# Kernel tuning notes

Hardware: AMD Instinct MI355X
Metric: run time of the kernel (lower is better)

Reference implementation:

```python
import jax, jax.numpy as jnp
import numpy as np

B, L, IN_DIM, D_MODEL = 4, 1024, 128, 256
MDIM = 2 * D_MODEL          # mamba_dim = 512 (must equal 2*d_model for shape consistency)
NL = 4                      # mamba_layers
DIN = 2 * MDIM              # d_inner (expand=2)
NST = 16                    # d_state
DTR = MDIM // 16            # dt_rank = 32
KC = 4                      # d_conv
EPS = 1e-5

# sinusoidal positional encoding buffer (deterministic)
_pos = np.arange(L, dtype=np.float32)[:, None]
_div = np.exp(np.arange(0, MDIM, 2, dtype=np.float32) * (-np.log(10000.0) / MDIM))
_pe = np.zeros((L, MDIM), dtype=np.float32)
_pe[:, 0::2] = np.sin(_pos * _div)
_pe[:, 1::2] = np.cos(_pos * _div)
PE = jnp.asarray(_pe)


def setup_inputs() -> dict:
    key = jax.random.key(0)
    ks = iter(jax.random.split(key, 64))
    rn = lambda shape, s=0.02: jax.random.normal(next(ks), shape, jnp.float32) * s
    inp = {
        "x": jax.random.normal(next(ks), (B, L, IN_DIM), jnp.float32),
        "rtg": jax.random.normal(next(ks), (B, L, 1), jnp.float32),
        "state_emb_w": rn((D_MODEL, IN_DIM)), "state_emb_b": jnp.zeros((D_MODEL,)),
        "reward_emb_w": rn((D_MODEL, 1)), "reward_emb_b": jnp.zeros((D_MODEL,)),
        "ln_w": jnp.ones((MDIM,)), "ln_b": jnp.zeros((MDIM,)),
        "in_proj_w": rn((NL, 2 * DIN, MDIM)),
        "conv_w": rn((NL, DIN, KC), 0.1), "conv_b": jnp.zeros((NL, DIN)),
        "x_proj_w": rn((NL, DTR + 2 * NST, DIN)),
        "dt_proj_w": rn((NL, DIN, DTR), 0.1), "dt_proj_b": jnp.full((NL, DIN), -2.0),
        "A_log": jnp.tile(jnp.log(jnp.arange(1, NST + 1, dtype=jnp.float32)), (NL, DIN, 1)),
        "D_param": jnp.ones((NL, DIN)),
        "out_proj_w": rn((NL, MDIM, DIN)),
        "norm_w": jnp.ones((NL, MDIM)), "norm_f_w": jnp.ones((MDIM,)),
        "so_w1": rn((MDIM // 2, MDIM)), "so_b1": jnp.zeros((MDIM // 2,)),
        "so_w2": rn((IN_DIM, MDIM // 2)), "so_b2": jnp.zeros((IN_DIM,)),
        "ro_w1": rn((MDIM // 2, MDIM)), "ro_b1": jnp.zeros((MDIM // 2,)),
        "ro_w2": rn((1, MDIM // 2)), "ro_b2": jnp.zeros((1,)),
    }
    return inp


def _rmsnorm(h, w):
    return h * jax.lax.rsqrt(jnp.mean(h * h, -1, keepdims=True) + EPS) * w


def _mamba(h, ipw, cw, cb, xpw, dpw, dpb, Alog, Dp, opw):
    # h: [B,L,MDIM]
    Ls = h.shape[1]
    xz = h @ ipw.T                                   # [B,L,2*DIN]
    xx, z = jnp.split(xz, 2, axis=-1)
    # causal depthwise conv, kernel KC, left pad KC-1
    xp = jnp.pad(xx, ((0, 0), (KC - 1, 0), (0, 0)))
    xc = cb + sum(cw[:, k] * xp[:, k:k + Ls, :] for k in range(KC))
    xc = jax.nn.silu(xc)                             # [B,L,DIN]
    dbc = xc @ xpw.T                                 # [B,L,DTR+2*NST]
    dt = jax.nn.softplus(dbc[..., :DTR] @ dpw.T + dpb)   # [B,L,DIN]
    Bm = dbc[..., DTR:DTR + NST]                     # [B,L,NST]
    Cm = dbc[..., DTR + NST:]                        # [B,L,NST]
    A = -jnp.exp(Alog)                               # [DIN,NST]

    def step(hc, inp):
        dt_t, B_t, C_t, x_t = inp                    # [B,DIN],[B,NST],[B,NST],[B,DIN]
        hc = jnp.exp(dt_t[:, :, None] * A) * hc + (dt_t * x_t)[:, :, None] * B_t[:, None, :]
        return hc, jnp.einsum('bdn,bn->bd', hc, C_t)

    h0 = jnp.zeros((h.shape[0], DIN, NST), h.dtype)
    _, ys = jax.lax.scan(step, h0, (dt.swapaxes(0, 1), Bm.swapaxes(0, 1),
                                    Cm.swapaxes(0, 1), xc.swapaxes(0, 1)))
    y = ys.swapaxes(0, 1) + Dp * xc
    y = y * jax.nn.silu(z)
    return y @ opw.T                                 # [B,L,MDIM]


def _forward(x, rtg, state_emb_w, state_emb_b, reward_emb_w, reward_emb_b, ln_w, ln_b,
             in_proj_w, conv_w, conv_b, x_proj_w, dt_proj_w, dt_proj_b, A_log, D_param,
             out_proj_w, norm_w, norm_f_w, so_w1, so_b1, so_w2, so_b2, ro_w1, ro_b1, ro_w2, ro_b2):
    se = x @ state_emb_w.T + state_emb_b            # [B,L,D_MODEL]
    re = rtg @ reward_emb_w.T + reward_emb_b        # [B,L,D_MODEL]
    h = jnp.concatenate([se, re], axis=-1)          # [B,L,MDIM]
    h = h + PE[:h.shape[1]]                          # dropout is identity at eval
    mu = jnp.mean(h, -1, keepdims=True)
    var = jnp.var(h, -1, keepdims=True)
    h = (h - mu) * jax.lax.rsqrt(var + EPS) * ln_w + ln_b
    residual = None
    for i in range(NL):
        residual = h if residual is None else h + residual
        hn = _rmsnorm(residual, norm_w[i])
        h = _mamba(hn, in_proj_w[i], conv_w[i], conv_b[i], x_proj_w[i],
                   dt_proj_w[i], dt_proj_b[i], A_log[i], D_param[i], out_proj_w[i])
    residual = h + residual
    h = _rmsnorm(residual, norm_f_w)
    next_state = jax.nn.relu(h @ so_w1.T + so_b1) @ so_w2.T + so_b2   # [B,L,IN_DIM]
    next_reward = jax.nn.relu(h @ ro_w1.T + ro_b1) @ ro_w2.T + ro_b2  # [B,L,1]
    return next_state, next_reward


def reference(x, rtg, state_emb_w, state_emb_b, reward_emb_w, reward_emb_b, ln_w, ln_b,
              in_proj_w, conv_w, conv_b, x_proj_w, dt_proj_w, dt_proj_b, A_log, D_param,
              out_proj_w, norm_w, norm_f_w, so_w1, so_b1, so_w2, so_b2, ro_w1, ro_b1, ro_w2, ro_b2):
    return _forward(x, rtg, state_emb_w, state_emb_b, reward_emb_w, reward_emb_b, ln_w, ln_b,
                    in_proj_w, conv_w, conv_b, x_proj_w, dt_proj_w, dt_proj_b, A_log, D_param,
                    out_proj_w, norm_w, norm_f_w, so_w1, so_b1, so_w2, so_b2, ro_w1, ro_b1, ro_w2, ro_b2)
```

## Files before the change

### kernel.cpp

```cpp
#include <hip/hip_runtime.h>
#include <stdint.h>

typedef unsigned short u16;
typedef __attribute__((ext_vector_type(8))) short bf16x8;
typedef __attribute__((ext_vector_type(4))) float f32x4;

static __device__ __forceinline__ u16 f2b(float f) {
  uint32_t u = __builtin_bit_cast(uint32_t, f);
  u += 0x7fffu + ((u >> 16) & 1u);
  return (u16)(u >> 16);
}
static __device__ __forceinline__ float b2f(u16 h) {
  uint32_t u = ((uint32_t)h) << 16;
  return __builtin_bit_cast(float, u);
}

#define GLDS16(gsrc, ldst)                                                        \
  __builtin_amdgcn_global_load_lds(                                               \
      (const __attribute__((address_space(1))) void*)(gsrc),                      \
      (__attribute__((address_space(3))) void*)(ldst), 16, 0, 0)

__global__ void f2b_kernel(const float* __restrict__ in, u16* __restrict__ out, int n) {
  int i = blockIdx.x * 256 + threadIdx.x;
  if (i < n) out[i] = f2b(in[i]);
}

__global__ __launch_bounds__(256) void pe_kernel(float* __restrict__ PEt) {
  const int l = blockIdx.x;
  const float c = -9.210340371976184f / 512.f;
#pragma unroll
  for (int q = 0; q < 2; ++q) {
    int dd = threadIdx.x + q * 256;
    float div = expf((float)(2 * (dd >> 1)) * c);
    float v = (dd & 1) ? cosf((float)l * div) : sinf((float)l * div);
    PEt[(size_t)l * 512 + dd] = v;
  }
}

__global__ __launch_bounds__(256) void dpw_t_kernel(const float* __restrict__ dpw,
                                                    float* __restrict__ dpwT) {
  const int l = blockIdx.y;
  int idx = blockIdx.x * 256 + threadIdx.x;
  int j = idx >> 10, dd = idx & 1023;
  dpwT[(size_t)l * 32768 + idx] = dpw[(size_t)l * 32768 + (size_t)dd * 32 + j];
}

__global__ __launch_bounds__(256) void embed_ln2(
    const float* __restrict__ x, const float* __restrict__ rtg,
    const float* __restrict__ Wse, const float* __restrict__ bse,
    const float* __restrict__ Wre, const float* __restrict__ bre,
    const float* __restrict__ lnw, const float* __restrict__ lnb,
    const float* __restrict__ PEt, float* __restrict__ h) {
  const int tid = threadIdx.x;
  const int tok0 = blockIdx.x * 16;
  const int l0 = tok0 & 1023;
  __shared__ float xs[16][128];
  __shared__ float rt[16];
  __shared__ float sw[16][2][4];
  for (int i = tid; i < 16 * 128; i += 256) ((float*)xs)[i] = x[(size_t)tok0 * 128 + i];
  if (tid < 16) rt[tid] = rtg[tok0 + tid];
  __syncthreads();
  const int d = tid;
  float acc[16];
#pragma unroll
  for (int tt = 0; tt < 16; ++tt) acc[tt] = 0.f;
  const float* wrow = Wse + (size_t)d * 128;
  for (int k0 = 0; k0 < 128; k0 += 8) {
    float4 wa = *(const float4*)(wrow + k0);
    float4 wb = *(const float4*)(wrow + k0 + 4);
#pragma unroll
    for (int tt = 0; tt < 16; ++tt) {
      const float* xr = &xs[tt][k0];
      acc[tt] += xr[0] * wa.x + xr[1] * wa.y + xr[2] * wa.z + xr[3] * wa.w +
                 xr[4] * wb.x + xr[5] * wb.y + xr[6] * wb.z + xr[7] * wb.w;
    }
  }
  const float seb = bse[d], reW = Wre[d], reB = bre[d];
  const int lane = tid & 63, wv = tid >> 6;
  float h1a[16];
#pragma unroll
  for (int tt = 0; tt < 16; ++tt) {
    float h0 = acc[tt] + seb + PEt[(size_t)(l0 + tt) * 512 + d];
    float h1 = reB + rt[tt] * reW + PEt[(size_t)(l0 + tt) * 512 + 256 + d];
    acc[tt] = h0;
    h1a[tt] = h1;
    float s = h0 + h1, q = h0 * h0 + h1 * h1;
#pragma unroll
    for (int o = 32; o; o >>= 1) { s += __shfl_xor(s, o); q += __shfl_xor(q, o); }
    if (lane == 0) { sw[tt][0][wv] = s; sw[tt][1][wv] = q; }
  }
  __syncthreads();
#pragma unroll
  for (int tt = 0; tt < 16; ++tt) {
    float S = sw[tt][0][0] + sw[tt][0][1] + sw[tt][0][2] + sw[tt][0][3];
    float Q = sw[tt][1][0] + sw[tt][1][1] + sw[tt][1][2] + sw[tt][1][3];
    float mean = S * (1.f / 512.f);
    float var = Q * (1.f / 512.f) - mean * mean;
    float rstd = rsqrtf(var + 1e-5f);
    size_t base = (size_t)(tok0 + tt) * 512;
    h[base + d]       = (acc[tt] - mean) * rstd * lnw[d] + lnb[d];
    h[base + 256 + d] = (h1a[tt] - mean) * rstd * lnw[256 + d] + lnb[256 + d];
  }
}

__global__ __launch_bounds__(256) void resid_rms_kernel(
    const float* __restrict__ hin, float* __restrict__ residual,
    const float* __restrict__ w, u16* __restrict__ outb, int first) {
  const int tok = blockIdx.x;
  const int t = threadIdx.x;
  __shared__ float rq[4];
  size_t base = (size_t)tok * 512;
  float v0 = hin[base + t], v1 = hin[base + t + 256];
  if (!first) { v0 += residual[base + t]; v1 += residual[base + t + 256]; }
  residual[base + t] = v0;
  residual[base + t + 256] = v1;
  float q = v0 * v0 + v1 * v1;
#pragma unroll
  for (int o = 32; o; o >>= 1) q += __shfl_xor(q, o);
  if ((t & 63) == 0) rq[t >> 6] = q;
  __syncthreads();
  float Q = rq[0] + rq[1] + rq[2] + rq[3];
  float scale = rsqrtf(Q * (1.f / 512.f) + 1e-5f);
  outb[base + t]       = f2b(v0 * scale * w[t]);
  outb[base + t + 256] = f2b(v1 * scale * w[t + 256]);
}

template <int BM, int BN, int WM, int WN, int EPI>
__global__ __launch_bounds__(256) void gemm_bt(
    const u16* __restrict__ A, const u16* __restrict__ Bw,
    float* __restrict__ Cf, u16* __restrict__ Cb,
    const float* __restrict__ bias, int M, int N, int K) {
  constexpr int MF = BM / (WM * 16);
  constexpr int NF = BN / (WN * 16);
  constexpr int NCA = (BM * 4) / 256;
  constexpr int NCB = (BN * 4) / 256;
  __shared__ __align__(16) u16 lA[BM * 32];
  __shared__ __align__(16) u16 lB[BN * 32];
  const int tid = threadIdx.x;
  const int lane = tid & 63;
  const int wv = tid >> 6;
  const int wr = wv / WN, wc = wv % WN;
  const int m0 = blockIdx.x * BM, n0 = blockIdx.y * BN;
  const int kchunk = K / gridDim.z;
  const int kb = blockIdx.z * kchunk;

  f32x4 acc[MF][NF];
#pragma unroll
  for (int i = 0; i < MF; ++i)
#pragma unroll
    for (int j = 0; j < NF; ++j) acc[i][j] = (f32x4){0.f, 0.f, 0.f, 0.f};

  const int srow = tid >> 2, sck = tid & 3;
  const u16* Ag = A + (size_t)(m0 + srow) * K + sck * 8 + kb;
  const u16* Bg = Bw + (size_t)(n0 + srow) * K + sck * 8 + kb;

  for (int k0 = 0; k0 < kchunk; k0 += 32) {
#pragma unroll
    for (int it = 0; it < NCA; ++it)
      GLDS16(Ag + (size_t)it * 64 * K + k0, &lA[(it * 256 + tid) * 8]);
#pragma unroll
    for (int it = 0; it < NCB; ++it)
      GLDS16(Bg + (size_t)it * 64 * K + k0, &lB[(it * 256 + tid) * 8]);
    __syncthreads();
    bf16x8 af[MF], bfr[NF];
    const int koff = (lane >> 4) * 8;
#pragma unroll
    for (int mi = 0; mi < MF; ++mi) {
      int r = wr * (MF * 16) + mi * 16 + (lane & 15);
      af[mi] = *(const bf16x8*)(&lA[r * 32 + koff]);
    }
#pragma unroll
    for (int ni = 0; ni < NF; ++ni) {
      int r = wc * (NF * 16) + ni * 16 + (lane & 15);
      bfr[ni] = *(const bf16x8*)(&lB[r * 32 + koff]);
    }
#pragma unroll
    for (int mi = 0; mi < MF; ++mi)
#pragma unroll
      for (int ni = 0; ni < NF; ++ni)
        acc[mi][ni] = __builtin_amdgcn_mfma_f32_16x16x32_bf16(af[mi], bfr[ni], acc[mi][ni], 0, 0, 0);
    __syncthreads();
  }

  float* co = Cf + (size_t)blockIdx.z * (size_t)M * N;
  const int rbase = (lane >> 4) * 4;
  const int cbase = lane & 15;
#pragma unroll
  for (int mi = 0; mi < MF; ++mi) {
#pragma unroll
    for (int ni = 0; ni < NF; ++ni) {
      int row = m0 + wr * (MF * 16) + mi * 16 + rbase;
      int col = n0 + wc * (NF * 16) + ni * 16 + cbase;
      float bv = (EPI >= 2) ? bias[col] : 0.f;
#pragma unroll
      for (int r = 0; r < 4; ++r) {
        float v = acc[mi][ni][r] + bv;
        if (EPI == 2) v = fmaxf(v, 0.f);
        size_t idx = (size_t)(row + r) * N + col;
        if (EPI == 1 || EPI == 2) Cb[idx] = f2b(v);
        else co[idx] = v;
      }
    }
  }
}

__global__ __launch_bounds__(256) void conv_silu_kernel(
    const u16* __restrict__ xz, const float* __restrict__ cw,
    const float* __restrict__ cb, float* __restrict__ xc, u16* __restrict__ xcb) {
  int idx = blockIdx.x * 256 + threadIdx.x;
  int d = idx & 1023;
  int t = (idx >> 10) & 1023;
  int token = idx >> 10;
  float4 w4 = *(const float4*)(cw + (size_t)d * 4);
  const float wk[4] = {w4.x, w4.y, w4.z, w4.w};
  float s = cb[d];
  const u16* xx = xz + (size_t)(token - t) * 2048 + d;
#pragma unroll
  for (int k = 0; k < 4; ++k) {
    int tt = t - 3 + k;
    if (tt >= 0) s += wk[k] * b2f(xx[(size_t)tt * 2048]);
  }
  float sl = s / (1.f + expf(-s));
  xc[idx] = sl;
  xcb[idx] = f2b(sl);
}

__global__ __launch_bounds__(256) void dt_kernel2(
    const float* __restrict__ P, const float* __restrict__ dpwT,
    const float* __restrict__ dpb, float* __restrict__ dtout,
    float* __restrict__ dbcr) {
  const int tid = threadIdx.x;
  const int tok0 = blockIdx.x * 16;
  __shared__ float sm[16][64];
  const size_t str = (size_t)4096 * 64;
  for (int i = tid; i < 16 * 64; i += 256) {
    size_t o = (size_t)tok0 * 64 + i;
    float v = P[o] + P[str + o] + P[2 * str + o] + P[3 * str + o];
    ((float*)sm)[i] = v;
    dbcr[o] = v;
  }
  __syncthreads();
  float acc0[16], acc1[16], acc2[16], acc3[16];
#pragma unroll
  for (int t = 0; t < 16; ++t) { acc0[t] = 0.f; acc1[t] = 0.f; acc2[t] = 0.f; acc3[t] = 0.f; }
#pragma unroll 4
  for (int j = 0; j < 32; ++j) {
    float w0 = dpwT[(size_t)j * 1024 + tid];
    float w1 = dpwT[(size_t)j * 1024 + 256 + tid];
    float w2 = dpwT[(size_t)j * 1024 + 512 + tid];
    float w3 = dpwT[(size_t)j * 1024 + 768 + tid];
#pragma unroll
    for (int t = 0; t < 16; ++t) {
      float sv = sm[t][j];
      acc0[t] += sv * w0;
      acc1[t] += sv * w1;
      acc2[t] += sv * w2;
      acc3[t] += sv * w3;
    }
  }
  const float b0 = dpb[tid], b1 = dpb[256 + tid], b2 = dpb[512 + tid], b3 = dpb[768 + tid];
#pragma unroll
  for (int t = 0; t < 16; ++t) {
    size_t o = (size_t)(tok0 + t) * 1024 + tid;
    float a0 = acc0[t] + b0, a1 = acc1[t] + b1, a2 = acc2[t] + b2, a3 = acc3[t] + b3;
    dtout[o]       = (a0 > 20.f) ? a0 : logf(1.f + expf(a0));
    dtout[o + 256] = (a1 > 20.f) ? a1 : logf(1.f + expf(a1));
    dtout[o + 512] = (a2 > 20.f) ? a2 : logf(1.f + expf(a2));
    dtout[o + 768] = (a3 > 20.f) ? a3 : logf(1.f + expf(a3));
  }
}

__global__ __launch_bounds__(256) void scan1(
    const float* __restrict__ dt, const float* __restrict__ xc,
    const float* __restrict__ dbc, const float* __restrict__ Alog,
    float* __restrict__ Ebuf, float* __restrict__ Ubuf, int NCc, int TCc) {
  const int d = blockIdx.x * 256 + threadIdx.x;
  const int c = blockIdx.y;
  const int b = blockIdx.z;
  const int t0 = c * TCc;
  __shared__ __align__(16) float sB[64][16];
  for (int i = threadIdx.x; i < TCc * 16; i += 256) {
    int t = i >> 4, n = i & 15;
    sB[t][n] = dbc[((size_t)(b * 1024 + t0 + t)) * 64 + 32 + n];
  }
  float A2[16];
#pragma unroll
  for (int q = 0; q < 4; ++q) {
    float4 a4 = *(const float4*)(Alog + (size_t)d * 16 + q * 4);
    A2[q * 4 + 0] = -expf(a4.x) * 1.4426950408889634f;
    A2[q * 4 + 1] = -expf(a4.y) * 1.4426950408889634f;
    A2[q * 4 + 2] = -expf(a4.z) * 1.4426950408889634f;
    A2[q * 4 + 3] = -expf(a4.w) * 1.4426950408889634f;
  }
  __syncthreads();
  float hc[16];
#pragma unroll
  for (int n = 0; n < 16; ++n) hc[n] = 0.f;
  float sumdt = 0.f;
  size_t tok = (size_t)b * 1024 + t0;
  for (int t = 0; t < TCc; ++t, ++tok) {
    float dtv = dt[tok * 1024 + d];
    float xcv = xc[tok * 1024 + d];
    float du = dtv * xcv;
    sumdt += dtv;
#pragma unroll
    for (int q = 0; q < 4; ++q) {
      float4 B4 = *(const float4*)(&sB[t][q * 4]);
      float e0 = exp2f(dtv * A2[q * 4 + 0]);
      float e1 = exp2f(dtv * A2[q * 4 + 1]);
      float e2 = exp2f(dtv * A2[q * 4 + 2]);
      float e3 = exp2f(dtv * A2[q * 4 + 3]);
      hc[q * 4 + 0] = e0 * hc[q * 4 + 0] + du * B4.x;
      hc[q * 4 + 1] = e1 * hc[q * 4 + 1] + du * B4.y;
      hc[q * 4 + 2] = e2 * hc[q * 4 + 2] + du * B4.z;
      hc[q * 4 + 3] = e3 * hc[q * 4 + 3] + du * B4.w;
    }
  }
  size_t ob = (((size_t)b * NCc + c) * 16) * 1024 + d;
#pragma unroll
  for (int n = 0; n < 16; ++n) {
    Ebuf[ob + (size_t)n * 1024] = exp2f(A2[n] * sumdt);
    Ubuf[ob + (size_t)n * 1024] = hc[n];
  }
}

__global__ __launch_bounds__(256) void scan_mid(
    const float* __restrict__ Ebuf, const float* __restrict__ Ubuf,
    float* __restrict__ H0, int NCc) {
  int idx = blockIdx.x * 256 + threadIdx.x;
  int b = idx >> 14;
  int nd = idx & 16383;
  float h = 0.f;
  size_t o0 = ((size_t)b * NCc * 16) * 1024 + nd;
  const size_t cstr = (size_t)16 * 1024;
  for (int cc = 0; cc < NCc; ++cc) {
    size_t o = o0 + (size_t)cc * cstr;
    H0[o] = h;
    if (cc < NCc - 1) h = Ebuf[o] * h + Ubuf[o];
  }
}

__global__ __launch_bounds__(256) void scan2(
    const float* __restrict__ dt, const float* __restrict__ xc,
    const float* __restrict__ dbc, const u16* __restrict__ xz,
    const float* __restrict__ Alog, const float* __restrict__ Dp,
    const float* __restrict__ H0, u16* __restrict__ yg, int NCc, int TCc) {
  const int d = blockIdx.x * 256 + threadIdx.x;
  const int c = blockIdx.y;
  const int b = blockIdx.z;
  const int t0 = c * TCc;
  __shared__ __align__(16) float sB[64][16];
  __shared__ __align__(16) float sC[64][16];
  for (int i = threadIdx.x; i < TCc * 16; i += 256) {
    int t = i >> 4, n = i & 15;
    size_t o = ((size_t)(b * 1024 + t0 + t)) * 64 + 32;
    sB[t][n] = dbc[o + n];
    sC[t][n] = dbc[o + 16 + n];
  }
  float A2[16];
#pragma unroll
  for (int q = 0; q < 4; ++q) {
    float4 a4 = *(const float4*)(Alog + (size_t)d * 16 + q * 4);
    A2[q * 4 + 0] = -expf(a4.x) * 1.4426950408889634f;
    A2[q * 4 + 1] = -expf(a4.y) * 1.4426950408889634f;
    A2[q * 4 + 2] = -expf(a4.z) * 1.4426950408889634f;
    A2[q * 4 + 3] = -expf(a4.w) * 1.4426950408889634f;
  }
  const float Dd = Dp[d];
  float hc[16];
  size_t ob = (((size_t)b * NCc + c) * 16) * 1024 + d;
#pragma unroll
  for (int n = 0; n < 16; ++n) hc[n] = H0[ob + (size_t)n * 1024];
  __syncthreads();
  size_t tok = (size_t)b * 1024 + t0;
  for (int t = 0; t < TCc; ++t, ++tok) {
    float dtv = dt[tok * 1024 + d];
    float xcv = xc[tok * 1024 + d];
    float du = dtv * xcv;
    float y0 = 0.f, y1 = 0.f, y2 = 0.f, y3 = 0.f;
#pragma unroll
    for (int q = 0; q < 4; ++q) {
      float4 B4 = *(const float4*)(&sB[t][q * 4]);
      float4 C4 = *(const float4*)(&sC[t][q * 4]);
      float e0 = exp2f(dtv * A2[q * 4 + 0]);
      float e1 = exp2f(dtv * A2[q * 4 + 1]);
      float e2 = exp2f(dtv * A2[q * 4 + 2]);
      float e3 = exp2f(dtv * A2[q * 4 + 3]);
      hc[q * 4 + 0] = e0 * hc[q * 4 + 0] + du * B4.x;
      hc[q * 4 + 1] = e1 * hc[q * 4 + 1] + du * B4.y;
      hc[q * 4 + 2] = e2 * hc[q * 4 + 2] + du * B4.z;
      hc[q * 4 + 3] = e3 * hc[q * 4 + 3] + du * B4.w;
      y0 += hc[q * 4 + 0] * C4.x;
      y1 += hc[q * 4 + 1] * C4.y;
      y2 += hc[q * 4 + 2] * C4.z;
      y3 += hc[q * 4 + 3] * C4.w;
    }
    float y = (y0 + y1) + (y2 + y3);
    float z = b2f(xz[tok * 2048 + 1024 + d]);
    float g = z / (1.f + expf(-z));
    yg[tok * 1024 + d] = f2b((y + Dd * xcv) * g);
  }
}

__global__ __launch_bounds__(256) void reward_head_kernel(
    const u16* __restrict__ t1r, const float* __restrict__ w2,
    const float* __restrict__ b2, float* __restrict__ outr) {
  int tok = blockIdx.x * 4 + (threadIdx.x >> 6);
  int lane = threadIdx.x & 63;
  float s = 0.f;
#pragma unroll
  for (int j = 0; j < 256; j += 64) s += b2f(t1r[(size_t)tok * 256 + j + lane]) * w2[j + lane];
#pragma unroll
  for (int o = 32; o; o >>= 1) s += __shfl_xor(s, o);
  if (lane == 0) outr[tok] = s + b2[0];
}

extern "C" void kernel_launch(void* const* d_in, const int* in_sizes, int n_in,
                              void* d_out, int out_size, void* d_ws, size_t ws_size,
                              hipStream_t stream) {
  const float* x    = (const float*)d_in[0];
  const float* rtg  = (const float*)d_in[1];
  const float* Wse  = (const float*)d_in[2];
  const float* bse  = (const float*)d_in[3];
  const float* Wre  = (const float*)d_in[4];
  const float* bre  = (const float*)d_in[5];
  const float* lnw  = (const float*)d_in[6];
  const float* lnb  = (const float*)d_in[7];
  const float* ipw  = (const float*)d_in[8];
  const float* cw   = (const float*)d_in[9];
  const float* cb   = (const float*)d_in[10];
  const float* xpw  = (const float*)d_in[11];
  const float* dpw  = (const float*)d_in[12];
  const float* dpb  = (const float*)d_in[13];
  const float* Alog = (const float*)d_in[14];
  const float* Dp   = (const float*)d_in[15];
  const float* opw  = (const float*)d_in[16];
  const float* nw   = (const float*)d_in[17];
  const float* nfw  = (const float*)d_in[18];
  const float* sow1 = (const float*)d_in[19];
  const float* sob1 = (const float*)d_in[20];
  const float* sow2 = (const float*)d_in[21];
  const float* sob2 = (const float*)d_in[22];
  const float* row1 = (const float*)d_in[23];
  const float* rob1 = (const float*)d_in[24];
  const float* row2 = (const float*)d_in[25];
  const float* rob2 = (const float*)d_in[26];
  (void)in_sizes; (void)n_in; (void)out_size;

  char* wsp = (char*)d_ws;
  size_t off = 0;
  auto alloc = [&](size_t bytes) -> void* {
    off = (off + 255) & ~(size_t)255;
    void* p = wsp + off;
    off += bytes;
    return p;
  };
  const int TOK = 4096;
  float* h     = (float*)alloc((size_t)TOK * 512 * 4);
  float* resid = (float*)alloc((size_t)TOK * 512 * 4);
  u16* hn      = (u16*)alloc((size_t)TOK * 512 * 2);
  u16* xzb     = (u16*)alloc((size_t)TOK * 2048 * 2);
  float* xcf   = (float*)alloc((size_t)TOK * 1024 * 4);
  u16* xcb     = (u16*)alloc((size_t)TOK * 1024 * 2);
  float* dbcP  = (float*)alloc((size_t)4 * TOK * 64 * 4);
  float* dbc   = (float*)alloc((size_t)TOK * 64 * 4);
  float* dtf   = (float*)alloc((size_t)TOK * 1024 * 4);
  float* PEt   = (float*)alloc((size_t)1024 * 512 * 4);
  float* dpwT  = (float*)alloc((size_t)4 * 32 * 1024 * 4);
  u16* ipwb    = (u16*)alloc((size_t)4 * 2048 * 512 * 2);
  u16* xpwb    = (u16*)alloc((size_t)4 * 64 * 1024 * 2);
  u16* opwb    = (u16*)alloc((size_t)4 * 512 * 1024 * 2);
  u16* sow1b   = (u16*)alloc((size_t)256 * 512 * 2);
  u16* sow2b   = (u16*)alloc((size_t)128 * 256 * 2);
  u16* row1b   = (u16*)alloc((size_t)256 * 512 * 2);

  size_t base_off = (off + 255) & ~(size_t)255;
  auto scan_bytes = [](int nc) {
    return (size_t)3 * 4 * nc * 16 * 1024 * 4 + 512;
  };
  int NCc = 16;
  if (ws_size >= base_off + scan_bytes(64)) NCc = 64;
  else if (ws_size >= base_off + scan_bytes(32)) NCc = 32;
  int TCc = 1024 / NCc;
  char* shared8 = (char*)alloc((size_t)2 * 4096 * NCc * 16 * 4);
  float* Ebuf  = (float*)shared8;
  float* Ubuf  = Ebuf + (size_t)4096 * NCc * 16;
  float* H0    = (float*)alloc((size_t)4096 * NCc * 16 * 4);
  u16* t1s     = (u16*)shared8;
  u16* t1r     = t1s + (size_t)TOK * 256;

  auto cvt = [&](const float* src, u16* dst, int n) {
    f2b_kernel<<<(n + 255) / 256, 256, 0, stream>>>(src, dst, n);
  };
  cvt(ipw, ipwb, 4 * 2048 * 512);
  cvt(xpw, xpwb, 4 * 64 * 1024);
  cvt(opw, opwb, 4 * 512 * 1024);
  cvt(sow1, sow1b, 256 * 512);
  cvt(sow2, sow2b, 128 * 256);
  cvt(row1, row1b, 256 * 512);

  pe_kernel<<<1024, 256, 0, stream>>>(PEt);
  dpw_t_kernel<<<dim3(128, 4), 256, 0, stream>>>(dpw, dpwT);
  embed_ln2<<<256, 256, 0, stream>>>(x, rtg, Wse, bse, Wre, bre, lnw, lnb, PEt, h);

  for (int i = 0; i < 4; ++i) {
    resid_rms_kernel<<<TOK, 256, 0, stream>>>(h, resid, nw + i * 512, hn, i == 0);
    gemm_bt<128, 128, 2, 2, 1><<<dim3(32, 16, 1), 256, 0, stream>>>(
        hn, ipwb + (size_t)i * 2048 * 512, nullptr, xzb, nullptr, 4096, 2048, 512);
    conv_silu_kernel<<<TOK * 1024 / 256, 256, 0, stream>>>(
        xzb, cw + (size_t)i * 4096, cb + i * 1024, xcf, xcb);
    gemm_bt<128, 64, 2, 2, 0><<<dim3(32, 1, 4), 256, 0, stream>>>(
        xcb, xpwb + (size_t)i * 64 * 1024, dbcP, nullptr, nullptr, 4096, 64, 1024);
    dt_kernel2<<<TOK / 16, 256, 0, stream>>>(dbcP, dpwT + (size_t)i * 32 * 1024,
                                             dpb + i * 1024, dtf, dbc);
    scan1<<<dim3(4, NCc - 1, 4), 256, 0, stream>>>(
        dtf, xcf, dbc, Alog + (size_t)i * 1024 * 16, Ebuf, Ubuf, NCc, TCc);
    scan_mid<<<256, 256, 0, stream>>>(Ebuf, Ubuf, H0, NCc);
    scan2<<<dim3(4, NCc, 4), 256, 0, stream>>>(
        dtf, xcf, dbc, xzb, Alog + (size_t)i * 1024 * 16, Dp + i * 1024,
        H0, xcb, NCc, TCc);
    gemm_bt<128, 64, 2, 2, 0><<<dim3(32, 8, 1), 256, 0, stream>>>(
        xcb, opwb + (size_t)i * 512 * 1024, h, nullptr, nullptr, 4096, 512, 1024);
  }

  resid_rms_kernel<<<TOK, 256, 0, stream>>>(h, resid, nfw, hn, 0);
  gemm_bt<64, 64, 2, 2, 2><<<dim3(64, 4, 1), 256, 0, stream>>>(
      hn, sow1b, nullptr, t1s, sob1, 4096, 256, 512);
  gemm_bt<64, 64, 2, 2, 3><<<dim3(64, 2, 1), 256, 0, stream>>>(
      t1s, sow2b, (float*)d_out, nullptr, sob2, 4096, 128, 256);
  gemm_bt<64, 64, 2, 2, 2><<<dim3(64, 4, 1), 256, 0, stream>>>(
      hn, row1b, nullptr, t1r, rob1, 4096, 256, 512);
  reward_head_kernel<<<TOK / 4, 256, 0, stream>>>(
      t1r, row2, rob2, (float*)d_out + (size_t)TOK * 128);
}
```

Measured before the change: 721.0 us.

## Store dt and conv output in bf16, recompute chunk decay, vectorize conv, merge casts

The dt and conv/SiLU activations are now stored only as bf16. The fp32 xc and dt buffers are gone, and both scan kernels read the bf16 versions, which roughly halves their per-token activation traffic. scan1 no longer writes a per-state decay buffer; it writes one sum of dt per chunk, and scan_mid recomputes the exponential from A_log. The conv kernel processes 8 channels per thread with vector loads and stores, and the six weight-conversion launches are merged into one kernel. In exchange, dt and the scan input lose precision, and scan2 now reads and writes the same bf16 buffer in place.

```diff
diff --git a/kernel.cpp b/kernel.cpp
--- a/kernel.cpp
+++ b/kernel.cpp
@@ -3,6 +3,7 @@
 
 typedef unsigned short u16;
 typedef __attribute__((ext_vector_type(8))) short bf16x8;
+typedef __attribute__((ext_vector_type(8))) u16 u16x8;
 typedef __attribute__((ext_vector_type(4))) float f32x4;
 
 static __device__ __forceinline__ u16 f2b(float f) {
@@ -20,9 +21,21 @@
       (const __attribute__((address_space(1))) void*)(gsrc),                      \
       (__attribute__((address_space(3))) void*)(ldst), 16, 0, 0)
 
-__global__ void f2b_kernel(const float* __restrict__ in, u16* __restrict__ out, int n) {
+__global__ __launch_bounds__(256) void cvt6_kernel(
+    const float* __restrict__ a0, u16* __restrict__ b0,
+    const float* __restrict__ a1, u16* __restrict__ b1,
+    const float* __restrict__ a2, u16* __restrict__ b2,
+    const float* __restrict__ a3, u16* __restrict__ b3,
+    const float* __restrict__ a4, u16* __restrict__ b4,
+    const float* __restrict__ a5, u16* __restrict__ b5) {
   int i = blockIdx.x * 256 + threadIdx.x;
-  if (i < n) out[i] = f2b(in[i]);
+  const int n0 = 4194304, n1 = 262144, n2 = 2097152, n3 = 131072, n4 = 32768, n5 = 131072;
+  if (i < n0) { b0[i] = f2b(a0[i]); return; } i -= n0;
+  if (i < n1) { b1[i] = f2b(a1[i]); return; } i -= n1;
+  if (i < n2) { b2[i] = f2b(a2[i]); return; } i -= n2;
+  if (i < n3) { b3[i] = f2b(a3[i]); return; } i -= n3;
+  if (i < n4) { b4[i] = f2b(a4[i]); return; } i -= n4;
+  if (i < n5) { b5[i] = f2b(a5[i]); }
 }
 
 __global__ __launch_bounds__(256) void pe_kernel(float* __restrict__ PEt) {
@@ -204,30 +217,38 @@
   }
 }
 
-__global__ __launch_bounds__(256) void conv_silu_kernel(
+__global__ __launch_bounds__(256) void conv_silu_kernel2(
     const u16* __restrict__ xz, const float* __restrict__ cw,
-    const float* __restrict__ cb, float* __restrict__ xc, u16* __restrict__ xcb) {
-  int idx = blockIdx.x * 256 + threadIdx.x;
-  int d = idx & 1023;
-  int t = (idx >> 10) & 1023;
-  int token = idx >> 10;
-  float4 w4 = *(const float4*)(cw + (size_t)d * 4);
-  const float wk[4] = {w4.x, w4.y, w4.z, w4.w};
-  float s = cb[d];
-  const u16* xx = xz + (size_t)(token - t) * 2048 + d;
+    const float* __restrict__ cb, u16* __restrict__ xcb) {
+  int gid = blockIdx.x * 256 + threadIdx.x;
+  int d0 = (gid & 127) * 8;
+  int token = gid >> 7;
+  int t = token & 1023;
+  const u16* xx = xz + (size_t)(token - t) * 2048 + d0;
+  float s[8];
+#pragma unroll
+  for (int j = 0; j < 8; ++j) s[j] = cb[d0 + j];
 #pragma unroll
   for (int k = 0; k < 4; ++k) {
     int tt = t - 3 + k;
-    if (tt >= 0) s += wk[k] * b2f(xx[(size_t)tt * 2048]);
-  }
-  float sl = s / (1.f + expf(-s));
-  xc[idx] = sl;
-  xcb[idx] = f2b(sl);
+    if (tt >= 0) {
+      u16x8 v = *(const u16x8*)(xx + (size_t)tt * 2048);
+#pragma unroll
+      for (int j = 0; j < 8; ++j) s[j] += cw[(size_t)(d0 + j) * 4 + k] * b2f(v[j]);
+    }
+  }
+  u16x8 o;
+#pragma unroll
+  for (int j = 0; j < 8; ++j) {
+    float sl = s[j] / (1.f + expf(-s[j]));
+    o[j] = f2b(sl);
+  }
+  *(u16x8*)(xcb + (size_t)token * 1024 + d0) = o;
 }
 
 __global__ __launch_bounds__(256) void dt_kernel2(
     const float* __restrict__ P, const float* __restrict__ dpwT,
-    const float* __restrict__ dpb, float* __restrict__ dtout,
+    const float* __restrict__ dpb, u16* __restrict__ dtout,
     float* __restrict__ dbcr) {
   const int tid = threadIdx.x;
   const int tok0 = blockIdx.x * 16;
@@ -263,17 +284,17 @@
   for (int t = 0; t < 16; ++t) {
     size_t o = (size_t)(tok0 + t) * 1024 + tid;
     float a0 = acc0[t] + b0, a1 = acc1[t] + b1, a2 = acc2[t] + b2, a3 = acc3[t] + b3;
-    dtout[o]       = (a0 > 20.f) ? a0 : logf(1.f + expf(a0));
-    dtout[o + 256] = (a1 > 20.f) ? a1 : logf(1.f + expf(a1));
-    dtout[o + 512] = (a2 > 20.f) ? a2 : logf(1.f + expf(a2));
-    dtout[o + 768] = (a3 > 20.f) ? a3 : logf(1.f + expf(a3));
+    dtout[o]       = f2b((a0 > 20.f) ? a0 : logf(1.f + expf(a0)));
+    dtout[o + 256] = f2b((a1 > 20.f) ? a1 : logf(1.f + expf(a1)));
+    dtout[o + 512] = f2b((a2 > 20.f) ? a2 : logf(1.f + expf(a2)));
+    dtout[o + 768] = f2b((a3 > 20.f) ? a3 : logf(1.f + expf(a3)));
   }
 }
 
 __global__ __launch_bounds__(256) void scan1(
-    const float* __restrict__ dt, const float* __restrict__ xc,
+    const u16* __restrict__ dt, const u16* __restrict__ xc,
     const float* __restrict__ dbc, const float* __restrict__ Alog,
-    float* __restrict__ Ebuf, float* __restrict__ Ubuf, int NCc, int TCc) {
+    float* __restrict__ Ubuf, float* __restrict__ SD, int NCc, int TCc) {
   const int d = blockIdx.x * 256 + threadIdx.x;
   const int c = blockIdx.y;
   const int b = blockIdx.z;
@@ -299,8 +320,8 @@
   float sumdt = 0.f;
   size_t tok = (size_t)b * 1024 + t0;
   for (int t = 0; t < TCc; ++t, ++tok) {
-    float dtv = dt[tok * 1024 + d];
-    float xcv = xc[tok * 1024 + d];
+    float dtv = b2f(dt[tok * 1024 + d]);
+    float xcv = b2f(xc[tok * 1024 + d]);
     float du = dtv * xcv;
     sumdt += dtv;
 #pragma unroll
@@ -318,30 +339,34 @@
   }
   size_t ob = (((size_t)b * NCc + c) * 16) * 1024 + d;
 #pragma unroll
-  for (int n = 0; n < 16; ++n) {
-    Ebuf[ob + (size_t)n * 1024] = exp2f(A2[n] * sumdt);
-    Ubuf[ob + (size_t)n * 1024] = hc[n];
-  }
+  for (int n = 0; n < 16; ++n) Ubuf[ob + (size_t)n * 1024] = hc[n];
+  SD[((size_t)b * NCc + c) * 1024 + d] = sumdt;
 }
 
 __global__ __launch_bounds__(256) void scan_mid(
-    const float* __restrict__ Ebuf, const float* __restrict__ Ubuf,
-    float* __restrict__ H0, int NCc) {
+    const float* __restrict__ Ubuf, const float* __restrict__ SD,
+    const float* __restrict__ Alog, float* __restrict__ H0, int NCc) {
   int idx = blockIdx.x * 256 + threadIdx.x;
   int b = idx >> 14;
   int nd = idx & 16383;
+  int n = nd >> 10, d = nd & 1023;
+  const float A2 = -expf(Alog[(size_t)d * 16 + n]) * 1.4426950408889634f;
   float h = 0.f;
   size_t o0 = ((size_t)b * NCc * 16) * 1024 + nd;
   const size_t cstr = (size_t)16 * 1024;
+  size_t sd0 = ((size_t)b * NCc) * 1024 + d;
   for (int cc = 0; cc < NCc; ++cc) {
     size_t o = o0 + (size_t)cc * cstr;
     H0[o] = h;
-    if (cc < NCc - 1) h = Ebuf[o] * h + Ubuf[o];
+    if (cc < NCc - 1) {
+      float e = exp2f(A2 * SD[sd0 + (size_t)cc * 1024]);
+      h = e * h + Ubuf[o];
+    }
   }
 }
 
 __global__ __launch_bounds__(256) void scan2(
-    const float* __restrict__ dt, const float* __restrict__ xc,
+    const u16* __restrict__ dt, const u16* __restrict__ xc,
     const float* __restrict__ dbc, const u16* __restrict__ xz,
     const float* __restrict__ Alog, const float* __restrict__ Dp,
     const float* __restrict__ H0, u16* __restrict__ yg, int NCc, int TCc) {
@@ -374,8 +399,8 @@
   __syncthreads();
   size_t tok = (size_t)b * 1024 + t0;
   for (int t = 0; t < TCc; ++t, ++tok) {
-    float dtv = dt[tok * 1024 + d];
-    float xcv = xc[tok * 1024 + d];
+    float dtv = b2f(dt[tok * 1024 + d]);
+    float xcv = b2f(xc[tok * 1024 + d]);
     float du = dtv * xcv;
     float y0 = 0.f, y1 = 0.f, y2 = 0.f, y3 = 0.f;
 #pragma unroll
@@ -460,11 +485,10 @@
   float* resid = (float*)alloc((size_t)TOK * 512 * 4);
   u16* hn      = (u16*)alloc((size_t)TOK * 512 * 2);
   u16* xzb     = (u16*)alloc((size_t)TOK * 2048 * 2);
-  float* xcf   = (float*)alloc((size_t)TOK * 1024 * 4);
   u16* xcb     = (u16*)alloc((size_t)TOK * 1024 * 2);
   float* dbcP  = (float*)alloc((size_t)4 * TOK * 64 * 4);
   float* dbc   = (float*)alloc((size_t)TOK * 64 * 4);
-  float* dtf   = (float*)alloc((size_t)TOK * 1024 * 4);
+  u16* dtb     = (u16*)alloc((size_t)TOK * 1024 * 2);
   float* PEt   = (float*)alloc((size_t)1024 * 512 * 4);
   float* dpwT  = (float*)alloc((size_t)4 * 32 * 1024 * 4);
   u16* ipwb    = (u16*)alloc((size_t)4 * 2048 * 512 * 2);
@@ -476,29 +500,21 @@
 
   size_t base_off = (off + 255) & ~(size_t)255;
   auto scan_bytes = [](int nc) {
-    return (size_t)3 * 4 * nc * 16 * 1024 * 4 + 512;
+    return (size_t)2 * 4 * nc * 16 * 1024 * 4 + (size_t)4 * nc * 1024 * 4 + 1024;
   };
   int NCc = 16;
   if (ws_size >= base_off + scan_bytes(64)) NCc = 64;
   else if (ws_size >= base_off + scan_bytes(32)) NCc = 32;
   int TCc = 1024 / NCc;
-  char* shared8 = (char*)alloc((size_t)2 * 4096 * NCc * 16 * 4);
-  float* Ebuf  = (float*)shared8;
-  float* Ubuf  = Ebuf + (size_t)4096 * NCc * 16;
+  char* shared8 = (char*)alloc((size_t)4096 * NCc * 16 * 4);
+  float* Ubuf  = (float*)shared8;
   float* H0    = (float*)alloc((size_t)4096 * NCc * 16 * 4);
+  float* SD    = (float*)alloc((size_t)4 * NCc * 1024 * 4);
   u16* t1s     = (u16*)shared8;
   u16* t1r     = t1s + (size_t)TOK * 256;
 
-  auto cvt = [&](const float* src, u16* dst, int n) {
-    f2b_kernel<<<(n + 255) / 256, 256, 0, stream>>>(src, dst, n);
-  };
-  cvt(ipw, ipwb, 4 * 2048 * 512);
-  cvt(xpw, xpwb, 4 * 64 * 1024);
-  cvt(opw, opwb, 4 * 512 * 1024);
-  cvt(sow1, sow1b, 256 * 512);
-  cvt(sow2, sow2b, 128 * 256);
-  cvt(row1, row1b, 256 * 512);
-
+  cvt6_kernel<<<26752, 256, 0, stream>>>(ipw, ipwb, xpw, xpwb, opw, opwb,
+                                         sow1, sow1b, sow2, sow2b, row1, row1b);
   pe_kernel<<<1024, 256, 0, stream>>>(PEt);
   dpw_t_kernel<<<dim3(128, 4), 256, 0, stream>>>(dpw, dpwT);
   embed_ln2<<<256, 256, 0, stream>>>(x, rtg, Wse, bse, Wre, bre, lnw, lnb, PEt, h);
@@ -507,17 +523,17 @@
     resid_rms_kernel<<<TOK, 256, 0, stream>>>(h, resid, nw + i * 512, hn, i == 0);
     gemm_bt<128, 128, 2, 2, 1><<<dim3(32, 16, 1), 256, 0, stream>>>(
         hn, ipwb + (size_t)i * 2048 * 512, nullptr, xzb, nullptr, 4096, 2048, 512);
-    conv_silu_kernel<<<TOK * 1024 / 256, 256, 0, stream>>>(
-        xzb, cw + (size_t)i * 4096, cb + i * 1024, xcf, xcb);
+    conv_silu_kernel2<<<2048, 256, 0, stream>>>(
+        xzb, cw + (size_t)i * 4096, cb + i * 1024, xcb);
     gemm_bt<128, 64, 2, 2, 0><<<dim3(32, 1, 4), 256, 0, stream>>>(
         xcb, xpwb + (size_t)i * 64 * 1024, dbcP, nullptr, nullptr, 4096, 64, 1024);
     dt_kernel2<<<TOK / 16, 256, 0, stream>>>(dbcP, dpwT + (size_t)i * 32 * 1024,
-                                             dpb + i * 1024, dtf, dbc);
+                                             dpb + i * 1024, dtb, dbc);
     scan1<<<dim3(4, NCc - 1, 4), 256, 0, stream>>>(
-        dtf, xcf, dbc, Alog + (size_t)i * 1024 * 16, Ebuf, Ubuf, NCc, TCc);
-    scan_mid<<<256, 256, 0, stream>>>(Ebuf, Ubuf, H0, NCc);
+        dtb, xcb, dbc, Alog + (size_t)i * 1024 * 16, Ubuf, SD, NCc, TCc);
+    scan_mid<<<256, 256, 0, stream>>>(Ubuf, SD, Alog + (size_t)i * 1024 * 16, H0, NCc);
     scan2<<<dim3(4, NCc, 4), 256, 0, stream>>>(
-        dtf, xcf, dbc, xzb, Alog + (size_t)i * 1024 * 16, Dp + i * 1024,
+        dtb, xcb, dbc, xzb, Alog + (size_t)i * 1024 * 16, Dp + i * 1024,
         H0, xcb, NCc, TCc);
     gemm_bt<128, 64, 2, 2, 0><<<dim3(32, 8, 1), 256, 0, stream>>>(
         xcb, opwb + (size_t)i * 512 * 1024, h, nullptr, nullptr, 4096, 512, 1024);
```

New measurement: 776.9 us, median of 2. 1.08x slower.
